# Kernel optimization log

Hardware: AMD Instinct MI355X
Metric: run time of the kernel (lower is better)

## Reference

```python
import jax, jax.numpy as jnp
import numpy as np

EPS = 1e-8


def setup_inputs() -> dict:
    key = jax.random.key(0)
    k0, k1, k2, k3 = jax.random.split(key, 4)
    b, cin, cout, h, w, kk, cond = 16, 512, 512, 64, 64, 3, 512
    return {
        "x": jax.random.normal(k0, (b, cin, h, w), jnp.float32),
        "y": jax.random.normal(k1, (b, cond), jnp.float32),
        "w_conv": jax.random.normal(k2, (cout, cin, kk, kk), jnp.float32) * 0.05,
        "w_gamma": jax.random.normal(k3, (cin, cond), jnp.float32) * 0.05,
        "b_gamma": jnp.ones((cin,), jnp.float32),
    }


def reference(x, y, w_conv, w_gamma, b_gamma):
    # fc_gamma: per-sample per-input-channel modulation scale  [b, cin]
    gamma = y @ w_gamma.T + b_gamma
    # modulate: [b, cout, cin, kh, kw]
    weight = w_conv[None, :, :, :, :] * gamma[:, None, :, None, None]
    # demodulate: rsqrt of sum over (cin, kh, kw) per (b, cout)
    d = jax.lax.rsqrt(jnp.sum(weight * weight, axis=(2, 3, 4), keepdims=True) + EPS)
    weight = weight * d

    # per-sample conv (equivalent to groups=b grouped conv), stride 1, same padding
    def conv_one(xi, wi):
        # xi: [cin, h, w], wi: [cout, cin, kh, kw]
        out = jax.lax.conv_general_dilated(
            xi[None], wi, window_strides=(1, 1), padding=[(1, 1), (1, 1)],
            dimension_numbers=("NCHW", "OIHW", "NCHW"))
        return out[0]

    return jax.vmap(conv_one)(x, weight)  # [b, cout, h, w]
```

## Files before the change

### kernel.cpp

```cpp
#include <hip/hip_runtime.h>
#include <stdint.h>

#define NB   16
#define CIN  512
#define COUT 512
#define HH   64
#define WW   64
#define NCOND 512
#define TAPS 9
#define EPSD 1e-8f

typedef short bf16x8 __attribute__((ext_vector_type(8)));
typedef float f32x4 __attribute__((ext_vector_type(4)));

static __device__ __forceinline__ short f2bf(float f) {
  union { float f; uint32_t u; } c;
  c.f = f;
  uint32_t u = c.u;
  uint32_t r = (u + 0x7FFFu + ((u >> 16) & 1u)) >> 16;
  return (short)(uint16_t)r;
}

static __device__ __forceinline__ void gl_lds16(const void* g, void* l) {
  __builtin_amdgcn_global_load_lds(
      (const __attribute__((address_space(1))) void*)g,
      (__attribute__((address_space(3))) void*)l, 16, 0, 0);
}

__global__ __launch_bounds__(512) void k_gamma(const float* __restrict__ y,
                                               const float* __restrict__ w_gamma,
                                               const float* __restrict__ b_gamma,
                                               float* __restrict__ gamma,
                                               float* __restrict__ zbuf) {
  __shared__ float ys[NCOND];
  const int b = blockIdx.x;
  const int i = threadIdx.x;
  if (zbuf && b == 0) { zbuf[i] = 0.f; zbuf[i + 512] = 0.f; }
  ys[i] = y[b * NCOND + i];
  __syncthreads();
  const float4* wg = reinterpret_cast<const float4*>(w_gamma + (size_t)i * NCOND);
  float acc = b_gamma[i];
  for (int c4 = 0; c4 < NCOND / 4; ++c4) {
    float4 w4 = wg[c4];
    acc += w4.x * ys[c4 * 4 + 0] + w4.y * ys[c4 * 4 + 1] +
           w4.z * ys[c4 * 4 + 2] + w4.w * ys[c4 * 4 + 3];
  }
  gamma[b * CIN + i] = acc;
}

__global__ __launch_bounds__(512) void k_d3(const float* __restrict__ gamma,
                                            const float* __restrict__ s2,
                                            float* __restrict__ dscale) {
  __shared__ float g2[CIN];
  __shared__ float red[512];
  const int b = blockIdx.x >> 3;
  const int og = blockIdx.x & 7;
  const int t = threadIdx.x;
  float g = gamma[b * CIN + t];
  g2[t] = g * g;
  __syncthreads();
  const int o_l = t >> 3, seg = t & 7;
  const int o = og * 64 + o_l;
  const float4* s4 = reinterpret_cast<const float4*>(s2 + (size_t)o * CIN + seg * 64);
  float p = 0.f;
#pragma unroll
  for (int c4 = 0; c4 < 16; ++c4) {
    float4 v = s4[c4];
    int base = seg * 64 + c4 * 4;
    p += v.x * g2[base + 0] + v.y * g2[base + 1] +
         v.z * g2[base + 2] + v.w * g2[base + 3];
  }
  red[t] = p;
  __syncthreads();
  if (seg == 0) {
    float s = 0.f;
#pragma unroll
    for (int k = 0; k < 8; ++k) s += red[o_l * 8 + k];
    dscale[b * COUT + o] = rsqrtf(s + EPSD);
  }
}

__global__ __launch_bounds__(256) void k_prep2(const float* __restrict__ w_conv,
                                               float* __restrict__ s2,
                                               short* __restrict__ W2) {
  __shared__ float ws_s[CIN * TAPS];
  const int o = blockIdx.x;
  const int t = threadIdx.x;
  const float* wsrc = w_conv + (size_t)o * CIN * TAPS;
  for (int idx = t; idx < CIN * TAPS; idx += 256) ws_s[idx] = wsrc[idx];
  __syncthreads();
  for (int i = t; i < CIN; i += 256) {
    float s = 0.f;
#pragma unroll
    for (int tap = 0; tap < TAPS; ++tap) {
      float v = ws_s[i * TAPS + tap];
      s += v * v;
    }
    s2[(size_t)o * CIN + i] = s;
  }
  const int key = (o >> 1) & 3;
  for (int k = t; k < CIN * TAPS; k += 256) {
    int tap = k >> 9;
    int r = k & 511;
    int c = r >> 5, sl = (r >> 3) & 3, j = r & 7;
    W2[((size_t)(c * TAPS + tap) * COUT + o) * 32 + ((sl ^ key) * 8) + j] =
        f2bf(ws_s[r * TAPS + tap]);
  }
}

__global__ __launch_bounds__(256) void k_prep(const float* __restrict__ w_conv,
                                              float* __restrict__ s2,
                                              short* __restrict__ Wr) {
  __shared__ float ws_s[CIN * TAPS];
  const int o = blockIdx.x;
  const int t = threadIdx.x;
  const float* wsrc = w_conv + (size_t)o * CIN * TAPS;
  for (int idx = t; idx < CIN * TAPS; idx += 256) ws_s[idx] = wsrc[idx];
  __syncthreads();
  for (int i = t; i < CIN; i += 256) {
    float s = 0.f;
#pragma unroll
    for (int tap = 0; tap < TAPS; ++tap) {
      float v = ws_s[i * TAPS + tap];
      s += v * v;
    }
    s2[(size_t)o * CIN + i] = s;
  }
  for (int idx = t; idx < CIN * TAPS; idx += 256) {
    int i = idx & (CIN - 1);
    int tap = idx >> 9;
    Wr[((size_t)o * TAPS + tap) * CIN + i] = f2bf(ws_s[i * TAPS + tap]);
  }
}

__global__ __launch_bounds__(512) void k_d(const float* __restrict__ gamma,
                                           const float* __restrict__ s2,
                                           float* __restrict__ dscale) {
  __shared__ float g2[CIN];
  const int b = blockIdx.x;
  const int o = threadIdx.x;
  float g = gamma[b * CIN + o];
  g2[o] = g * g;
  __syncthreads();
  const float4* s4 = reinterpret_cast<const float4*>(s2 + (size_t)o * CIN);
  float acc = 0.f;
  for (int i4 = 0; i4 < CIN / 4; ++i4) {
    float4 v = s4[i4];
    acc += v.x * g2[i4 * 4 + 0] + v.y * g2[i4 * 4 + 1] +
           v.z * g2[i4 * 4 + 2] + v.w * g2[i4 * 4 + 3];
  }
  dscale[b * COUT + o] = rsqrtf(acc + EPSD);
}

__global__ __launch_bounds__(256) void k_xmod2(const float* __restrict__ x,
                                               const float* __restrict__ gamma,
                                               short* __restrict__ xm) {
  __shared__ float tile[64][67];
  __shared__ float gs[CIN];
  const int y = blockIdx.x, b = blockIdx.y;
  const int t = threadIdx.x;
  gs[t] = gamma[b * CIN + t];
  gs[t + 256] = gamma[b * CIN + t + 256];
  __syncthreads();
  const int w = t >> 2, q = t & 3;
  const int sw = (w >> 1) & 3;
  short* dst = xm + (((size_t)b * HH + y) * WW + w) * CIN;
  for (int c0 = 0; c0 < CIN; c0 += 64) {
    {
      int ww_ = t & 63;
      int cb = t >> 6;
      const float* xp = x + (((size_t)(b * CIN + c0 + cb)) * HH + y) * WW + ww_;
#pragma unroll
      for (int p = 0; p < 16; ++p)
        tile[cb + p * 4][ww_] = xp[(size_t)p * 4 * HH * WW];
    }
    __syncthreads();
#pragma unroll
    for (int h = 0; h < 2; ++h) {
      int c_lo = q * 16 + h * 8;
      int chunk = (c0 + c_lo) >> 5;
      int sl = (c_lo >> 3) & 3;
      short tmp[8];
#pragma unroll
      for (int j = 0; j < 8; ++j)
        tmp[j] = f2bf(tile[c_lo + j][w] * gs[c0 + c_lo + j]);
      *reinterpret_cast<bf16x8*>(dst + chunk * 32 + (sl ^ sw) * 8) =
          *reinterpret_cast<const bf16x8*>(tmp);
    }
    __syncthreads();
  }
}

__global__ __launch_bounds__(256, 2) void k_conv12(const short* __restrict__ xm,
                                                   const short* __restrict__ W2,
                                                   const short* __restrict__ zbuf,
                                                   const float* __restrict__ dscale,
                                                   float* __restrict__ out) {
  __shared__ short Xs[2 * 6 * 64 * 32];
  __shared__ float d_s[128];
  __shared__ __align__(16) short zls[64];

  const int orig = blockIdx.x;
  const int wgid = ((orig & 7) << 7) | (orig >> 3);
  const int ot = wgid >> 8;
  const int b  = (wgid >> 4) & 15;
  const int sp = wgid & 15;

  const int t = threadIdx.x, lane = t & 63;
  const int wc = t >> 6;
  const int l15 = lane & 15;
  const int slA = lane >> 4;

  if (t < 128) d_s[t] = dscale[b * COUT + ot * 128 + t];
  if (t < 64) zls[t] = 0;

  const short* xS[6];
#pragma unroll
  for (int i = 0; i < 6; ++i) {
    int idx = t + 256 * i;
    int rb = idx >> 8;
    int w = (idx & 255) >> 2;
    int sl = idx & 3;
    int ysrc = sp * 4 + rb - 1;
    bool rv = (ysrc >= 0) && (ysrc < HH);
    xS[i] = rv ? xm + (((size_t)b * HH + ysrc) * WW + w) * CIN + sl * 8
               : zbuf + sl * 8;
  }

  const int o0 = ot * 128 + l15;
  const int keyA = (o0 >> 1) & 3;
  const short* aGc = W2 + (size_t)o0 * 32 + ((slA ^ keyA) * 8);

  const int kb0 = slA << 4;
  const char* pbx[3];
#pragma unroll
  for (int dxi = 0; dxi < 3; ++dxi) {
    int lcc = l15 + dxi - 1;
    int key = (lcc >> 1) & 3;
    pbx[dxi] = (const char*)&Xs[0] + lcc * 64 + (kb0 ^ (key << 4));
  }
  const int lc3 = (l15 + 1 > 15) ? 15 : (l15 + 1);
  const char* pbx3 = (const char*)&Xs[0] + lc3 * 64 + (kb0 ^ (((lc3 >> 1) & 3) << 4));
  char* wx0 = (char*)&Xs[0] + t * 16;
  const char* zl = (const char*)&zls[0];
  const bool mL = (l15 == 0);
  const bool mR = (l15 == 15);

  f32x4 acc[8][4];
#pragma unroll
  for (int m = 0; m < 8; ++m)
#pragma unroll
    for (int n = 0; n < 4; ++n)
      acc[m][n] = (f32x4){0.f, 0.f, 0.f, 0.f};

  bf16x8 aA[8], aB[8];

#pragma unroll
  for (int i = 0; i < 6; ++i)
    gl_lds16(xS[i], wx0 + i * 4096);
#pragma unroll
  for (int m = 0; m < 8; ++m)
    aA[m] = *reinterpret_cast<const bf16x8*>(aGc + m * 512);
  asm volatile("s_waitcnt vmcnt(0) lgkmcnt(0)" ::: "memory");
  __builtin_amdgcn_s_barrier();
  asm volatile("" ::: "memory");

#define DO_TAP(tp, CUR, NXT, NXTOFF, STGX, KNV)                               \
  {                                                                           \
    const short* an_ = aGc + (NXTOFF);                                        \
    _Pragma("unroll") for (int m_ = 0; m_ < 8; ++m_)                          \
        NXT[m_] = *reinterpret_cast<const bf16x8*>(an_ + m_ * 512);           \
    if (STGX) {                                                               \
      _Pragma("unroll") for (int i_ = 0; i_ < 6; ++i_)                        \
          gl_lds16(xS[i_] + (KNV), wxw + i_ * 4096);                          \
    }                                                                         \
    __builtin_amdgcn_sched_barrier(0);                                        \
    {                                                                         \
      const int dy_ = (tp) / 3 - 1, dx_ = (tp) % 3 - 1;                       \
      const int rbo_ = (wc + dy_ + 1) * 4096;                                 \
      bf16x8 bfr[4];                                                          \
      const char* qq_ = (dx_ == -1) ? qq0 : ((dx_ == 0) ? qq1 : qq2);         \
      const char* s0_ = (dx_ == -1 && mL) ? (zl - rbo_) : qq_;                \
      const char* s3_ = (dx_ == 1) ? (mR ? (zl - rbo_ - 3072) : qq3) : qq_;   \
      bfr[0] = *reinterpret_cast<const bf16x8*>(s0_ + rbo_);                  \
      bfr[1] = *reinterpret_cast<const bf16x8*>(qq_ + rbo_ + 1024);           \
      bfr[2] = *reinterpret_cast<const bf16x8*>(qq_ + rbo_ + 2048);           \
      bfr[3] = *reinterpret_cast<const bf16x8*>(s3_ + rbo_ + 3072);           \
      __builtin_amdgcn_s_setprio(1);                                          \
      _Pragma("unroll") for (int m_ = 0; m_ < 8; ++m_)                        \
        _Pragma("unroll") for (int n_ = 0; n_ < 4; ++n_)                      \
          acc[m_][n_] = __builtin_amdgcn_mfma_f32_16x16x32_bf16(              \
              CUR[m_], bfr[n_], acc[m_][n_], 0, 0, 0);                        \
      __builtin_amdgcn_s_setprio(0);                                          \
    }                                                                         \
  }

#define CHUNK_TAPS(A0, A1, NX8, KNV)                                          \
  DO_TAP(0, A0, A1, 16384, false, 0)                                          \
  DO_TAP(1, A1, A0, 32768, false, 0)                                          \
  DO_TAP(2, A0, A1, 49152, false, 0)                                          \
  DO_TAP(3, A1, A0, 65536, false, 0)                                          \
  DO_TAP(4, A0, A1, 81920, false, 0)                                          \
  DO_TAP(5, A1, A0, 98304, false, 0)                                          \
  DO_TAP(6, A0, A1, 114688, false, 0)                                         \
  DO_TAP(7, A1, A0, 131072, true, KNV)                                        \
  DO_TAP(8, A0, A1, (NX8), false, 0)                                          \
  __builtin_amdgcn_sched_barrier(0);                                          \
  asm volatile("s_waitcnt vmcnt(8)" ::: "memory");                            \
  __builtin_amdgcn_s_barrier();                                               \
  asm volatile("" ::: "memory");

  for (int c2 = 0; c2 < 8; ++c2) {
    {
      const char* qq0 = pbx[0];
      const char* qq1 = pbx[1];
      const char* qq2 = pbx[2];
      const char* qq3 = pbx3;
      char* wxw = wx0 + 24576;
      const int knv = (2 * c2 + 1) * 32;
      CHUNK_TAPS(aA, aB, 147456, knv)
    }
    aGc += 147456;
    {
      const char* qq0 = pbx[0] + 24576;
      const char* qq1 = pbx[1] + 24576;
      const char* qq2 = pbx[2] + 24576;
      const char* qq3 = pbx3 + 24576;
      char* wxw = wx0;
      const int knv = (c2 < 7) ? (2 * c2 + 2) * 32 : 0;
      const int nx8 = (c2 < 7) ? 147456 : 0;
      CHUNK_TAPS(aB, aA, nx8, knv)
    }
    aGc += 147456;
  }
#undef CHUNK_TAPS
#undef DO_TAP

#pragma unroll
  for (int m = 0; m < 8; ++m) {
#pragma unroll
    for (int n = 0; n < 4; ++n) {
#pragma unroll
      for (int j = 0; j < 4; ++j) {
        int o_l = m * 16 + (lane >> 4) * 4 + j;
        int o = ot * 128 + o_l;
        int yy = sp * 4 + wc;
        int cx = n * 16 + l15;
        out[(((size_t)b * COUT + o) * HH + yy) * WW + cx] = d_s[o_l] * acc[m][n][j];
      }
    }
  }
}

__global__ __launch_bounds__(256) void k_conv_fb(const float* __restrict__ x,
                                                 const short* __restrict__ Wr,
                                                 const float* __restrict__ gamma,
                                                 const float* __restrict__ dscale,
                                                 float* __restrict__ out) {
  __shared__ short As[128 * 64];
  __shared__ short Xs[4 * 64 * 64];
  __shared__ float gam_s[CIN];
  __shared__ float d_s[128];

  const int sp = blockIdx.x;
  const int ot = blockIdx.y;
  const int b  = blockIdx.z;
  const int t  = threadIdx.x;
  const int lane = t & 63;
  const int wv = t >> 6;
  const int wr = wv >> 1;
  const int wc = wv & 1;

  gam_s[t] = gamma[b * CIN + t];
  gam_s[t + 256] = gamma[b * CIN + t + 256];
  if (t < 128) d_s[t] = dscale[b * COUT + ot * 128 + t];

  f32x4 acc[4][4];
#pragma unroll
  for (int m = 0; m < 4; ++m)
#pragma unroll
    for (int n = 0; n < 4; ++n)
      acc[m][n] = (f32x4){0.f, 0.f, 0.f, 0.f};

  const int srow = t >> 6;
  const int sc = t & 63;
  const int ysrc = sp * 2 + srow - 1;
  const bool rv = (ysrc >= 0) && (ysrc < HH);
  const int ycl = rv ? ysrc : 0;
  const float* xrow = x + (((size_t)b * CIN) * HH + ycl) * WW + sc;
  short* xs_base = &Xs[(srow * 64 + sc) * 64];
  const int xs_sw = (sc & 7) << 4;

  for (int chunk = 0; chunk < CIN / 64; ++chunk) {
    const int i0 = chunk * 64;
    __syncthreads();
    {
      const float* xp = xrow + (size_t)i0 * (HH * WW);
#pragma unroll
      for (int i8 = 0; i8 < 8; ++i8) {
        short tmp[8];
#pragma unroll
        for (int j = 0; j < 8; ++j) {
          int i = i8 * 8 + j;
          float v = rv ? xp[i * (HH * WW)] : 0.0f;
          tmp[j] = f2bf(v * gam_s[i0 + i]);
        }
        char* dst = (char*)xs_base + ((i8 * 16) ^ xs_sw);
        *reinterpret_cast<bf16x8*>(dst) = *reinterpret_cast<const bf16x8*>(tmp);
      }
    }
    for (int tap = 0; tap < TAPS; ++tap) {
      __syncthreads();
#pragma unroll
      for (int j = 0; j < 4; ++j) {
        int s = t + 256 * j;
        int row = s >> 3, sl = s & 7;
        int kbyte = (sl * 16) ^ ((row & 7) << 4);
        const short* src = Wr + ((size_t)(ot * 128 + row) * TAPS + tap) * CIN +
                           i0 + (kbyte >> 1);
        *reinterpret_cast<bf16x8*>((char*)As + row * 128 + sl * 16) =
            *reinterpret_cast<const bf16x8*>(src);
      }
      __syncthreads();

      const int dy = tap / 3 - 1, dx = tap % 3 - 1;
      bf16x8 afr[2][4], bfr[2][4];
#pragma unroll
      for (int kk = 0; kk < 2; ++kk) {
        const int kb = kk * 64 + (lane >> 4) * 16;
#pragma unroll
        for (int m = 0; m < 4; ++m) {
          int row = wr * 64 + m * 16 + (lane & 15);
          afr[kk][m] = *reinterpret_cast<const bf16x8*>(
              (const char*)As + row * 128 + (kb ^ ((row & 7) << 4)));
        }
#pragma unroll
        for (int n = 0; n < 4; ++n) {
          int p = wc * 64 + n * 16 + (lane & 15);
          int r = p >> 6, c = p & 63;
          int cc = c + dx;
          bool val = (cc >= 0) && (cc < WW);
          int ccl = val ? cc : 0;
          int rr = r + dy + 1;
          bf16x8 f = *reinterpret_cast<const bf16x8*>(
              (const char*)Xs + (rr * 64 + ccl) * 128 + (kb ^ ((ccl & 7) << 4)));
          if (!val) f = (bf16x8){0, 0, 0, 0, 0, 0, 0, 0};
          bfr[kk][n] = f;
        }
      }
#pragma unroll
      for (int m = 0; m < 4; ++m)
#pragma unroll
        for (int n = 0; n < 4; ++n)
#pragma unroll
          for (int kk = 0; kk < 2; ++kk)
            acc[m][n] = __builtin_amdgcn_mfma_f32_16x16x32_bf16(
                afr[kk][m], bfr[kk][n], acc[m][n], 0, 0, 0);
    }
  }

#pragma unroll
  for (int m = 0; m < 4; ++m) {
#pragma unroll
    for (int n = 0; n < 4; ++n) {
#pragma unroll
      for (int j = 0; j < 4; ++j) {
        int o_l = wr * 64 + m * 16 + (lane >> 4) * 4 + j;
        int o = ot * 128 + o_l;
        int p = wc * 64 + n * 16 + (lane & 15);
        int yy = sp * 2 + (p >> 6);
        int cx = p & 63;
        out[(((size_t)b * COUT + o) * HH + yy) * WW + cx] = d_s[o_l] * acc[m][n][j];
      }
    }
  }
}

extern "C" void kernel_launch(void* const* d_in, const int* in_sizes, int n_in,
                              void* d_out, int out_size, void* d_ws, size_t ws_size,
                              hipStream_t stream) {
  const float* x = (const float*)d_in[0];
  const float* y = (const float*)d_in[1];
  const float* w_conv = (const float*)d_in[2];
  const float* w_gamma = (const float*)d_in[3];
  const float* b_gamma = (const float*)d_in[4];
  float* out = (float*)d_out;

  char* ws = (char*)d_ws;
  short* W2 = (short*)ws;
  float* gamma = (float*)(ws + 4849664);
  float* dsc = (float*)(ws + 4882432);
  float* s2 = (float*)(ws + 4915200);
  char* zbuf = ws + 5963776;
  short* xm = (short*)(ws + 5967872);
  const size_t NEED = 5967872 + (size_t)NB * HH * WW * CIN * 2 + 4096;

  const bool fast = ws_size >= NEED;

  if (fast) {
    hipLaunchKernelGGL(k_prep2, dim3(COUT), dim3(256), 0, stream, w_conv, s2, W2);
    hipLaunchKernelGGL(k_gamma, dim3(NB), dim3(512), 0, stream, y, w_gamma,
                       b_gamma, gamma, (float*)zbuf);
    hipLaunchKernelGGL(k_d3, dim3(128), dim3(512), 0, stream, gamma, s2, dsc);
    hipLaunchKernelGGL(k_xmod2, dim3(HH, NB), dim3(256), 0, stream, x, gamma, xm);
    hipLaunchKernelGGL(k_conv12, dim3(1024), dim3(256), 0, stream, xm, W2,
                       (const short*)zbuf, dsc, out);
  } else {
    hipLaunchKernelGGL(k_gamma, dim3(NB), dim3(512), 0, stream, y, w_gamma,
                       b_gamma, gamma, (float*)nullptr);
    hipLaunchKernelGGL(k_prep, dim3(COUT), dim3(256), 0, stream, w_conv, s2, W2);
    hipLaunchKernelGGL(k_d, dim3(NB), dim3(512), 0, stream, gamma, s2, dsc);
    hipLaunchKernelGGL(k_conv_fb, dim3(32, 4, NB), dim3(256), 0, stream, x, W2,
                       gamma, dsc, out);
  }
}
```

Before: 312.4 us.

## Software-pipeline B-fragment LDS reads across taps and fuse prep/gamma kernels

The conv kernel's inner tap loop now reads B fragments from LDS through a rolling three-entry register buffer. Each fragment is loaded three MFMA groups ahead, with fine-grained lgkmcnt waits, so LDS latency overlaps with MFMA work instead of stalling before each tap's 32 MFMAs. Separately, the weight-prep and gamma kernels are merged into one launch with 512+16 blocks of 512 threads, removing one launch and letting the small gamma blocks run beside the prep blocks. The hand-counted lgkmcnt waits are fragile if the compiler reorders or adds LDS operations.

After: 306.4 us, median of 3. About the same (-1.9%).

```diff
diff --git a/kernel.cpp b/kernel.cpp
--- a/kernel.cpp
+++ b/kernel.cpp
@@ -25,6 +25,87 @@
   __builtin_amdgcn_global_load_lds(
       (const __attribute__((address_space(1))) void*)g,
       (__attribute__((address_space(3))) void*)l, 16, 0, 0);
+}
+
+__global__ __launch_bounds__(512) void k_pg(const float* __restrict__ w_conv,
+                                            const float* __restrict__ y,
+                                            const float* __restrict__ w_gamma,
+                                            const float* __restrict__ b_gamma,
+                                            float* __restrict__ s2,
+                                            short* __restrict__ W2,
+                                            float* __restrict__ gamma,
+                                            float* __restrict__ zbuf) {
+  __shared__ float ws_s[CIN * TAPS];
+  const int t = threadIdx.x;
+  if (blockIdx.x < 512) {
+    const int o = blockIdx.x;
+    const float* wsrc = w_conv + (size_t)o * CIN * TAPS;
+    for (int idx = t; idx < CIN * TAPS; idx += 512) ws_s[idx] = wsrc[idx];
+    __syncthreads();
+    {
+      int i = t;
+      float s = 0.f;
+#pragma unroll
+      for (int tap = 0; tap < TAPS; ++tap) {
+        float v = ws_s[i * TAPS + tap];
+        s += v * v;
+      }
+      s2[(size_t)o * CIN + i] = s;
+    }
+    const int key = (o >> 1) & 3;
+    for (int k = t; k < CIN * TAPS; k += 512) {
+      int tap = k >> 9;
+      int r = k & 511;
+      int c = r >> 5, sl = (r >> 3) & 3, j = r & 7;
+      W2[((size_t)(c * TAPS + tap) * COUT + o) * 32 + ((sl ^ key) * 8) + j] =
+          f2bf(ws_s[r * TAPS + tap]);
+    }
+  } else {
+    const int b = blockIdx.x - 512;
+    if (b == 0) { zbuf[t] = 0.f; zbuf[t + 512] = 0.f; }
+    ws_s[t] = y[b * NCOND + t];
+    __syncthreads();
+    const float4* wg = reinterpret_cast<const float4*>(w_gamma + (size_t)t * NCOND);
+    float acc = b_gamma[t];
+    for (int c4 = 0; c4 < NCOND / 4; ++c4) {
+      float4 w4 = wg[c4];
+      acc += w4.x * ws_s[c4 * 4 + 0] + w4.y * ws_s[c4 * 4 + 1] +
+             w4.z * ws_s[c4 * 4 + 2] + w4.w * ws_s[c4 * 4 + 3];
+    }
+    gamma[b * CIN + t] = acc;
+  }
+}
+
+__global__ __launch_bounds__(512) void k_d3(const float* __restrict__ gamma,
+                                            const float* __restrict__ s2,
+                                            float* __restrict__ dscale) {
+  __shared__ float g2[CIN];
+  __shared__ float red[512];
+  const int b = blockIdx.x >> 3;
+  const int og = blockIdx.x & 7;
+  const int t = threadIdx.x;
+  float g = gamma[b * CIN + t];
+  g2[t] = g * g;
+  __syncthreads();
+  const int o_l = t >> 3, seg = t & 7;
+  const int o = og * 64 + o_l;
+  const float4* s4 = reinterpret_cast<const float4*>(s2 + (size_t)o * CIN + seg * 64);
+  float p = 0.f;
+#pragma unroll
+  for (int c4 = 0; c4 < 16; ++c4) {
+    float4 v = s4[c4];
+    int base = seg * 64 + c4 * 4;
+    p += v.x * g2[base + 0] + v.y * g2[base + 1] +
+         v.z * g2[base + 2] + v.w * g2[base + 3];
+  }
+  red[t] = p;
+  __syncthreads();
+  if (seg == 0) {
+    float s = 0.f;
+#pragma unroll
+    for (int k = 0; k < 8; ++k) s += red[o_l * 8 + k];
+    dscale[b * COUT + o] = rsqrtf(s + EPSD);
+  }
 }
 
 __global__ __launch_bounds__(512) void k_gamma(const float* __restrict__ y,
@@ -46,66 +127,6 @@
            w4.z * ys[c4 * 4 + 2] + w4.w * ys[c4 * 4 + 3];
   }
   gamma[b * CIN + i] = acc;
-}
-
-__global__ __launch_bounds__(512) void k_d3(const float* __restrict__ gamma,
-                                            const float* __restrict__ s2,
-                                            float* __restrict__ dscale) {
-  __shared__ float g2[CIN];
-  __shared__ float red[512];
-  const int b = blockIdx.x >> 3;
-  const int og = blockIdx.x & 7;
-  const int t = threadIdx.x;
-  float g = gamma[b * CIN + t];
-  g2[t] = g * g;
-  __syncthreads();
-  const int o_l = t >> 3, seg = t & 7;
-  const int o = og * 64 + o_l;
-  const float4* s4 = reinterpret_cast<const float4*>(s2 + (size_t)o * CIN + seg * 64);
-  float p = 0.f;
-#pragma unroll
-  for (int c4 = 0; c4 < 16; ++c4) {
-    float4 v = s4[c4];
-    int base = seg * 64 + c4 * 4;
-    p += v.x * g2[base + 0] + v.y * g2[base + 1] +
-         v.z * g2[base + 2] + v.w * g2[base + 3];
-  }
-  red[t] = p;
-  __syncthreads();
-  if (seg == 0) {
-    float s = 0.f;
-#pragma unroll
-    for (int k = 0; k < 8; ++k) s += red[o_l * 8 + k];
-    dscale[b * COUT + o] = rsqrtf(s + EPSD);
-  }
-}
-
-__global__ __launch_bounds__(256) void k_prep2(const float* __restrict__ w_conv,
-                                               float* __restrict__ s2,
-                                               short* __restrict__ W2) {
-  __shared__ float ws_s[CIN * TAPS];
-  const int o = blockIdx.x;
-  const int t = threadIdx.x;
-  const float* wsrc = w_conv + (size_t)o * CIN * TAPS;
-  for (int idx = t; idx < CIN * TAPS; idx += 256) ws_s[idx] = wsrc[idx];
-  __syncthreads();
-  for (int i = t; i < CIN; i += 256) {
-    float s = 0.f;
-#pragma unroll
-    for (int tap = 0; tap < TAPS; ++tap) {
-      float v = ws_s[i * TAPS + tap];
-      s += v * v;
-    }
-    s2[(size_t)o * CIN + i] = s;
-  }
-  const int key = (o >> 1) & 3;
-  for (int k = t; k < CIN * TAPS; k += 256) {
-    int tap = k >> 9;
-    int r = k & 511;
-    int c = r >> 5, sl = (r >> 3) & 3, j = r & 7;
-    W2[((size_t)(c * TAPS + tap) * COUT + o) * 32 + ((sl ^ key) * 8) + j] =
-        f2bf(ws_s[r * TAPS + tap]);
-  }
 }
 
 __global__ __launch_bounds__(256) void k_prep(const float* __restrict__ w_conv,
@@ -191,7 +212,7 @@
   }
 }
 
-__global__ __launch_bounds__(256, 2) void k_conv12(const short* __restrict__ xm,
+__global__ __launch_bounds__(256, 2) void k_conv13(const short* __restrict__ xm,
                                                    const short* __restrict__ W2,
                                                    const short* __restrict__ zbuf,
                                                    const float* __restrict__ dscale,
@@ -254,6 +275,7 @@
       acc[m][n] = (f32x4){0.f, 0.f, 0.f, 0.f};
 
   bf16x8 aA[8], aB[8];
+  bf16x8 bS[3];
 
 #pragma unroll
   for (int i = 0; i < 6; ++i)
@@ -265,37 +287,48 @@
   __builtin_amdgcn_s_barrier();
   asm volatile("" ::: "memory");
 
+#define LD8(p) (*reinterpret_cast<const bf16x8*>(p))
+
+#define ADDR_B(tq_, nq_)                                                      \
+  ({ const int dyz_ = (tq_) / 3 - 1, dxz_ = (tq_) % 3 - 1;                    \
+     const int rboz_ = (wc + dyz_ + 1) * 4096;                                \
+     const char* pz_;                                                         \
+     if (dxz_ == -1 && (nq_) == 0) pz_ = mL ? (zl - rboz_) : qq0;             \
+     else if (dxz_ == 1 && (nq_) == 3) pz_ = mR ? (zl - rboz_ - 3072) : qq3;  \
+     else pz_ = (dxz_ == -1) ? qq0 : ((dxz_ == 0) ? qq1 : qq2);               \
+     pz_ + rboz_ + (nq_) * 1024; })
+
 #define DO_TAP(tp, CUR, NXT, NXTOFF, STGX, KNV)                               \
   {                                                                           \
     const short* an_ = aGc + (NXTOFF);                                        \
     _Pragma("unroll") for (int m_ = 0; m_ < 8; ++m_)                          \
-        NXT[m_] = *reinterpret_cast<const bf16x8*>(an_ + m_ * 512);           \
+        NXT[m_] = LD8(an_ + m_ * 512);                                        \
     if (STGX) {                                                               \
       _Pragma("unroll") for (int i_ = 0; i_ < 6; ++i_)                        \
           gl_lds16(xS[i_] + (KNV), wxw + i_ * 4096);                          \
     }                                                                         \
-    __builtin_amdgcn_sched_barrier(0);                                        \
-    {                                                                         \
-      const int dy_ = (tp) / 3 - 1, dx_ = (tp) % 3 - 1;                       \
-      const int rbo_ = (wc + dy_ + 1) * 4096;                                 \
-      bf16x8 bfr[4];                                                          \
-      const char* qq_ = (dx_ == -1) ? qq0 : ((dx_ == 0) ? qq1 : qq2);         \
-      const char* s0_ = (dx_ == -1 && mL) ? (zl - rbo_) : qq_;                \
-      const char* s3_ = (dx_ == 1) ? (mR ? (zl - rbo_ - 3072) : qq3) : qq_;   \
-      bfr[0] = *reinterpret_cast<const bf16x8*>(s0_ + rbo_);                  \
-      bfr[1] = *reinterpret_cast<const bf16x8*>(qq_ + rbo_ + 1024);           \
-      bfr[2] = *reinterpret_cast<const bf16x8*>(qq_ + rbo_ + 2048);           \
-      bfr[3] = *reinterpret_cast<const bf16x8*>(s3_ + rbo_ + 3072);           \
+    _Pragma("unroll") for (int n_ = 0; n_ < 4; ++n_) {                        \
+      const int j_ = (tp) * 4 + n_;                                           \
+      if (j_ <= 33) { asm volatile("s_waitcnt lgkmcnt(2)" ::: "memory"); }    \
+      else if (j_ == 34) { asm volatile("s_waitcnt lgkmcnt(1)" ::: "memory"); } \
+      else { asm volatile("s_waitcnt lgkmcnt(0)" ::: "memory"); }             \
+      __builtin_amdgcn_sched_barrier(0);                                      \
       __builtin_amdgcn_s_setprio(1);                                          \
       _Pragma("unroll") for (int m_ = 0; m_ < 8; ++m_)                        \
-        _Pragma("unroll") for (int n_ = 0; n_ < 4; ++n_)                      \
-          acc[m_][n_] = __builtin_amdgcn_mfma_f32_16x16x32_bf16(              \
-              CUR[m_], bfr[n_], acc[m_][n_], 0, 0, 0);                        \
+        acc[m_][n_] = __builtin_amdgcn_mfma_f32_16x16x32_bf16(                \
+            CUR[m_], bS[j_ % 3], acc[m_][n_], 0, 0, 0);                       \
       __builtin_amdgcn_s_setprio(0);                                          \
+      if (j_ + 3 <= 35) {                                                     \
+        const int jn_ = j_ + 3, tr_ = jn_ >> 2, nr_ = jn_ & 3;                \
+        bS[jn_ % 3] = LD8(ADDR_B(tr_, nr_));                                  \
+      }                                                                       \
     }                                                                         \
   }
 
 #define CHUNK_TAPS(A0, A1, NX8, KNV)                                          \
+  bS[0] = LD8(ADDR_B(0, 0));                                                  \
+  bS[1] = LD8(ADDR_B(0, 1));                                                  \
+  bS[2] = LD8(ADDR_B(0, 2));                                                  \
   DO_TAP(0, A0, A1, 16384, false, 0)                                          \
   DO_TAP(1, A1, A0, 32768, false, 0)                                          \
   DO_TAP(2, A0, A1, 49152, false, 0)                                          \
@@ -335,6 +368,8 @@
   }
 #undef CHUNK_TAPS
 #undef DO_TAP
+#undef ADDR_B
+#undef LD8
 
 #pragma unroll
   for (int m = 0; m < 8; ++m) {
@@ -498,12 +533,11 @@
   const bool fast = ws_size >= NEED;
 
   if (fast) {
-    hipLaunchKernelGGL(k_prep2, dim3(COUT), dim3(256), 0, stream, w_conv, s2, W2);
-    hipLaunchKernelGGL(k_gamma, dim3(NB), dim3(512), 0, stream, y, w_gamma,
-                       b_gamma, gamma, (float*)zbuf);
+    hipLaunchKernelGGL(k_pg, dim3(512 + NB), dim3(512), 0, stream, w_conv, y,
+                       w_gamma, b_gamma, s2, W2, gamma, (float*)zbuf);
     hipLaunchKernelGGL(k_d3, dim3(128), dim3(512), 0, stream, gamma, s2, dsc);
     hipLaunchKernelGGL(k_xmod2, dim3(HH, NB), dim3(256), 0, stream, x, gamma, xm);
-    hipLaunchKernelGGL(k_conv12, dim3(1024), dim3(256), 0, stream, xm, W2,
+    hipLaunchKernelGGL(k_conv13, dim3(1024), dim3(256), 0, stream, xm, W2,
                        (const short*)zbuf, dsc, out);
   } else {
     hipLaunchKernelGGL(k_gamma, dim3(NB), dim3(512), 0, stream, y, w_gamma,
```
